# Performance work log

Measured on AMD Instinct MI355X. Metric: run time of the kernel, lower is better.

## Reference

```python
import jax, jax.numpy as jnp
import numpy as np

N_NODES = 100000
N_EDGES = 1600000
IN_CH, EDGE_DIM, HIDDEN, OUT_CH = 3, 3, 64, 1


def setup_inputs() -> dict:
    key = jax.random.key(0)
    ks = jax.random.split(key, 10)
    x = jax.random.normal(ks[0], (N_NODES, IN_CH), dtype=jnp.float32)
    edge_index = jax.random.randint(ks[1], (2, N_EDGES), 0, N_NODES, dtype=jnp.int64)
    edge_attr = jax.random.normal(ks[2], (N_EDGES, EDGE_DIM), dtype=jnp.float32)
    # Linear params (torch Linear: y = x @ W.T + b); we store W as (in, out)
    s1 = 1.0 / np.sqrt(IN_CH + EDGE_DIM)
    W1 = jax.random.uniform(ks[3], (IN_CH + EDGE_DIM, HIDDEN), jnp.float32, -s1, s1)
    b1 = jax.random.uniform(ks[4], (HIDDEN,), jnp.float32, -s1, s1)
    s2 = 1.0 / np.sqrt(HIDDEN + EDGE_DIM)
    W2 = jax.random.uniform(ks[5], (HIDDEN + EDGE_DIM, HIDDEN), jnp.float32, -s2, s2)
    b2 = jax.random.uniform(ks[6], (HIDDEN,), jnp.float32, -s2, s2)
    s3 = 1.0 / np.sqrt(HIDDEN)
    W3 = jax.random.uniform(ks[7], (HIDDEN, OUT_CH), jnp.float32, -s3, s3)
    b3 = jax.random.uniform(ks[8], (OUT_CH,), jnp.float32, -s3, s3)
    return {"x": x, "edge_index": edge_index, "edge_attr": edge_attr,
            "W1": W1, "b1": b1, "W2": W2, "b2": b2, "W3": W3, "b3": b3}


def _edge_conv(h, src, dst, edge_attr, W, b, n_nodes):
    # gather source node features, concat edge_attr, linear, scatter-add at dst
    msg = jnp.concatenate([h[src], edge_attr], axis=-1) @ W + b  # [E, out]
    return jax.ops.segment_sum(msg, dst, num_segments=n_nodes)   # [N, out]


def reference(x, edge_index, edge_attr, W1, b1, W2, b2, W3, b3):
    src, dst = edge_index[0], edge_index[1]  # PyG source_to_target: aggregate at edge_index[1]
    n = x.shape[0]
    h = jax.nn.relu(_edge_conv(x, src, dst, edge_attr, W1, b1, n))
    h = jax.nn.relu(_edge_conv(h, src, dst, edge_attr, W2, b2, n))
    return h @ W3 + b3  # (n_nodes, 1) anomaly logits
```

## Files before the change

### kernel.cpp

```cpp
#include <hip/hip_runtime.h>

#define N_NODES 100000
#define N_EDGES 1600000
#define NCHUNK 256
#define CHUNK_E (N_EDGES / NCHUNK)
#define BSHIFT 6
#define BMASK 63
#define NBUCK 1563
#define CAP 24
#define CSRB 1536
#define REC_CAP 1344


typedef unsigned int uint4_ev __attribute__((ext_vector_type(4)));
typedef short bf16x8 __attribute__((ext_vector_type(8)));
typedef float f32x4 __attribute__((ext_vector_type(4)));

__device__ __forceinline__ unsigned short f2bf(float f) {
    unsigned int u = __float_as_uint(f);
    unsigned int r = (u + 0x7fff + ((u >> 16) & 1)) >> 16;
    return (unsigned short)r;
}
__device__ __forceinline__ unsigned int pack2bf(float a, float b) {
    return (unsigned int)f2bf(a) | ((unsigned int)f2bf(b) << 16);
}
__device__ __forceinline__ float bflo(unsigned int v) { return __uint_as_float(v << 16); }
__device__ __forceinline__ float bfhi(unsigned int v) { return __uint_as_float(v & 0xffff0000u); }

__device__ __forceinline__ float4 nt_load4(const float4* p) {
    uint4_ev v = __builtin_nontemporal_load((const uint4_ev*)p);
    return make_float4(__uint_as_float(v.x), __uint_as_float(v.y),
                       __uint_as_float(v.z), __uint_as_float(v.w));
}

__device__ __forceinline__ int wave_incl_scan(int v, int lane) {
#pragma unroll
    for (int off = 1; off < 64; off <<= 1) {
        int t = __shfl_up(v, off, 64);
        if (lane >= off) v += t;
    }
    return v;
}

__global__ __launch_bounds__(1024) void k_scatter(const int* __restrict__ ei,
                                                  const float* __restrict__ ea,
                                                  const float* __restrict__ W2,
                                                  unsigned short* __restrict__ wpk,
                                                  const float* __restrict__ x,
                                                  float4* __restrict__ xp,
                                                  unsigned char* __restrict__ cnt8,
                                                  float4* __restrict__ stg) {
    const int g = blockIdx.x, t = threadIdx.x;
    if (g > NCHUNK) {
        int i = (g - NCHUNK - 1) * 1024 + t;
        if (i < N_NODES)
            xp[i] = make_float4(x[i * 3 + 0], x[i * 3 + 1], x[i * 3 + 2], 0.f);
        return;
    }
    if (g == NCHUNK) {
        if (t < 512) {
            int lane = t & 63, hh = (t >> 6) & 1, nt = t >> 7;
            int col = nt * 16 + (lane & 15);
            int k0 = hh * 32 + (lane >> 4) * 8;
#pragma unroll
            for (int j = 0; j < 8; j++)
                wpk[t * 8 + j] = f2bf(W2[(k0 + j) * 64 + col]);
        }
        return;
    }
    __shared__ int cur[NBUCK];
    for (int i = t; i < NBUCK; i += 1024) cur[i] = 0;
    const int base = g * CHUNK_E;
    int srcv[7], dstv[7];
    float a0v[7], a1v[7], a2v[7];
#pragma unroll
    for (int k = 0; k < 7; k++) {
        int i = t + k * 1024;
        if (i < CHUNK_E) {
            int e = base + i;
            srcv[k] = ei[e];
            dstv[k] = ei[N_EDGES + e];
            a0v[k] = ea[(size_t)e * 3 + 0];
            a1v[k] = ea[(size_t)e * 3 + 1];
            a2v[k] = ea[(size_t)e * 3 + 2];
        }
    }
    __syncthreads();
#pragma unroll
    for (int k = 0; k < 7; k++) {
        int i = t + k * 1024;
        if (i < CHUNK_E) {
            int bb = dstv[k] >> BSHIFT;
            int p = atomicAdd(&cur[bb], 1);
            if (p < CAP) {
                unsigned pk = (unsigned)srcv[k] | ((unsigned)(dstv[k] & BMASK) << 17);
                stg[((size_t)bb * NCHUNK + g) * CAP + p] =
                    make_float4(__uint_as_float(pk), a0v[k], a1v[k], a2v[k]);
            }
        }
    }
    __syncthreads();
    for (int i = t; i < NBUCK; i += 1024)
        cnt8[(size_t)g * NBUCK + i] = (unsigned char)min(cur[i], 255);
}

__global__ __launch_bounds__(512) void k_finalize(
    const float4* __restrict__ stg, const unsigned char* __restrict__ cnt8,
    const float4* __restrict__ xp, const float* __restrict__ W1,
    const float* __restrict__ b1, const float* __restrict__ W2,
    const float* __restrict__ b2, const bf16x8* __restrict__ wpk,
    int* __restrict__ csr, int* __restrict__ rowinfo,
    unsigned int* __restrict__ zu, unsigned int* __restrict__ eu) {
    __shared__ float4 rec[REC_CAP];
    __shared__ unsigned short stripof[REC_CAP];
    __shared__ int hist[64], lofs[64], curq[64];
    __shared__ float sU[64 * 3], sT[64 * 3];
    __shared__ int ws8[8];
    const int b = blockIdx.x, t = threadIdx.x;
    const int lane = t & 63, w = t >> 6;
    const int c = (t < NCHUNK) ? min((int)cnt8[(size_t)t * NBUCK + b], CAP) : 0;
    int inc = wave_incl_scan(c, lane);
    if (lane == 63) ws8[w] = inc;
    if (t < 64) hist[t] = 0;
    __syncthreads();
    int wo = 0;
#pragma unroll
    for (int k = 0; k < 8; k++) wo += (k < w) ? ws8[k] : 0;
    const int ex = wo + inc - c;
    int tot = 0;
#pragma unroll
    for (int k = 0; k < 8; k++) tot += ws8[k];
    const int cntb = min(tot, REC_CAP);
    for (int j = 0; j < c; ++j)
        if (ex + j < REC_CAP)
            stripof[ex + j] = (unsigned short)((t << 5) | j);
    __syncthreads();
    float4 r_[3];
#pragma unroll
    for (int k = 0; k < 3; k++) {
        int i = t + k * 512;
        if (i < cntb) {
            int sp = stripof[i];
            r_[k] = nt_load4(&stg[((size_t)b * NCHUNK + (sp >> 5)) * CAP + (sp & 31)]);
        }
    }
#pragma unroll
    for (int k = 0; k < 3; k++) {
        int i = t + k * 512;
        if (i < cntb) atomicAdd(&hist[__float_as_uint(r_[k].x) >> 17], 1);
    }
    __syncthreads();
    if (t < 64) {
        int v = hist[t];
        int in2 = wave_incl_scan(v, t);
        lofs[t] = in2 - v;
        curq[t] = in2 - v;
    }
    __syncthreads();
#pragma unroll
    for (int k = 0; k < 3; k++) {
        int i = t + k * 512;
        if (i < cntb) {
            int p = atomicAdd(&curq[__float_as_uint(r_[k].x) >> 17], 1);
            if (p < REC_CAP) rec[p] = r_[k];
        }
    }
    __syncthreads();
    {
        const int l = t >> 3, sub = t & 7;
        const int n = b * 64 + l;
        const int d = hist[l], lo = lofs[l];
        float u0 = 0, u1 = 0, u2 = 0, t0 = 0, t1 = 0, t2 = 0;
        for (int j = sub; j < d; j += 8) {
            float4 r = rec[lo + j];
            unsigned pk = __float_as_uint(r.x);
            int src = pk & 0x1FFFF;
            csr[b * CSRB + lo + j] = src;
            t0 += r.y; t1 += r.z; t2 += r.w;
            float4 xv = xp[src];
            u0 += xv.x; u1 += xv.y; u2 += xv.z;
        }
#pragma unroll
        for (int off = 1; off <= 4; off <<= 1) {
            u0 += __shfl_xor(u0, off, 64); u1 += __shfl_xor(u1, off, 64);
            u2 += __shfl_xor(u2, off, 64); t0 += __shfl_xor(t0, off, 64);
            t1 += __shfl_xor(t1, off, 64); t2 += __shfl_xor(t2, off, 64);
        }
        if (sub == 0) {
            sU[l * 3 + 0] = u0; sU[l * 3 + 1] = u1; sU[l * 3 + 2] = u2;
            sT[l * 3 + 0] = t0; sT[l * 3 + 1] = t1; sT[l * 3 + 2] = t2;
            if (n < N_NODES)
                rowinfo[n] = (int)(((unsigned)(b * CSRB + lo) << 8) | (unsigned)d);
        }
    }
    __syncthreads();
    if (w >= 4) return;
    const int tb = b * 64 + w * 16;
    if (tb >= N_NODES) return;
    const int col = lane & 15;
    const int q = lane >> 4;
    const int ln = w * 16 + col;
    const float d = (float)hist[ln];
    const float u0 = sU[ln * 3], u1 = sU[ln * 3 + 1], u2 = sU[ln * 3 + 2];
    const float t0 = sT[ln * 3], t1 = sT[ln * 3 + 1], t2 = sT[ln * 3 + 2];
    bf16x8 af[2];
#pragma unroll
    for (int h = 0; h < 2; h++) {
#pragma unroll
        for (int j = 0; j < 8; j++) {
            int cch = h * 32 + q * 8 + j;
            float a = d * b1[cch];
            a = fmaf(u0, W1[0 * 64 + cch], a);
            a = fmaf(u1, W1[1 * 64 + cch], a);
            a = fmaf(u2, W1[2 * 64 + cch], a);
            a = fmaf(t0, W1[3 * 64 + cch], a);
            a = fmaf(t1, W1[4 * 64 + cch], a);
            a = fmaf(t2, W1[5 * 64 + cch], a);
            af[h][j] = (short)f2bf(fmaxf(a, 0.f));
        }
    }
    f32x4 acc[4];
#pragma unroll
    for (int nt = 0; nt < 4; nt++) {
        bf16x8 b0 = wpk[(nt * 2 + 0) * 64 + lane];
        bf16x8 b1f = wpk[(nt * 2 + 1) * 64 + lane];
        f32x4 a = {0.f, 0.f, 0.f, 0.f};
        a = __builtin_amdgcn_mfma_f32_16x16x32_bf16(af[0], b0, a, 0, 0, 0);
        a = __builtin_amdgcn_mfma_f32_16x16x32_bf16(af[1], b1f, a, 0, 0, 0);
        acc[nt] = a;
    }
#pragma unroll
    for (int nt = 0; nt < 4; nt++) {
#pragma unroll
        for (int r = 0; r < 4; r++) {
            float v = acc[nt][r];
            float pv = __shfl_xor(v, 1, 64);
            if ((lane & 1) == 0) {
                int nr = tb + q * 4 + r;
                zu[(size_t)nr * 32 + nt * 8 + (col >> 1)] = pack2bf(v, pv);
            }
        }
    }
    const float eb = b2[lane];
    const float w64 = W2[64 * 64 + lane];
    const float w65 = W2[65 * 64 + lane];
    const float w66 = W2[66 * 64 + lane];
#pragma unroll 4
    for (int mm = 0; mm < 16; mm++) {
        int lm = w * 16 + mm;
        float dd = (float)hist[lm];
        float s0 = sT[lm * 3], s1 = sT[lm * 3 + 1], s2 = sT[lm * 3 + 2];
        float e = dd * eb;
        e = fmaf(s0, w64, e); e = fmaf(s1, w65, e); e = fmaf(s2, w66, e);
        float pe = __shfl_xor(e, 1, 64);
        if ((lane & 1) == 0)
            eu[(size_t)(tb + mm) * 32 + (lane >> 1)] = pack2bf(e, pe);
    }
}

__global__ __launch_bounds__(256) void k_agg(
    const unsigned int* __restrict__ zu, const unsigned int* __restrict__ eu,
    const int* __restrict__ rowinfo, const int* __restrict__ csr,
    const float* __restrict__ W3, const float* __restrict__ b3,
    float* __restrict__ out) {
    const int lane = threadIdx.x & 63;
    const int li = lane & 15;
    const int q = li & 7;
    const int r = li >> 3;
    const int n = blockIdx.x * 16 + (threadIdx.x >> 4);

    float cw3[8];
#pragma unroll
    for (int m = 0; m < 8; m++) cw3[m] = W3[8 * q + m];
    const float b3v = b3[0];

    const unsigned ri = (unsigned)rowinfo[n];
    const int start = (int)(ri >> 8), end = start + (int)(ri & 255u);
    float S[8];
#pragma unroll
    for (int m = 0; m < 8; m++) S[m] = 0.f;

    for (int c = start; c < end; c += 16) {
        int idx[8];
        float mk[8];
        uint4 v[8];
#pragma unroll
        for (int u = 0; u < 8; u++) {
            int i = c + 2 * u + r;
            bool ok = i < end;
            mk[u] = ok ? 1.f : 0.f;
            idx[u] = csr[ok ? i : start];
        }
#pragma unroll
        for (int u = 0; u < 8; u++)
            v[u] = *(const uint4*)&zu[(size_t)idx[u] * 32 + q * 4];
#pragma unroll
        for (int u = 0; u < 8; u++) {
            S[0] = fmaf(mk[u], bflo(v[u].x), S[0]); S[1] = fmaf(mk[u], bfhi(v[u].x), S[1]);
            S[2] = fmaf(mk[u], bflo(v[u].y), S[2]); S[3] = fmaf(mk[u], bfhi(v[u].y), S[3]);
            S[4] = fmaf(mk[u], bflo(v[u].z), S[4]); S[5] = fmaf(mk[u], bfhi(v[u].z), S[5]);
            S[6] = fmaf(mk[u], bflo(v[u].w), S[6]); S[7] = fmaf(mk[u], bfhi(v[u].w), S[7]);
        }
    }
#pragma unroll
    for (int m = 0; m < 8; m++) S[m] += __shfl_xor(S[m], 8, 64);

    const uint4 ev = *(const uint4*)&eu[(size_t)n * 32 + q * 4];
    float contrib;
    {
        float h0 = fmaxf(S[0] + bflo(ev.x), 0.f);
        float h1v = fmaxf(S[1] + bfhi(ev.x), 0.f);
        float h2v = fmaxf(S[2] + bflo(ev.y), 0.f);
        float h3 = fmaxf(S[3] + bfhi(ev.y), 0.f);
        float h4 = fmaxf(S[4] + bflo(ev.z), 0.f);
        float h5 = fmaxf(S[5] + bfhi(ev.z), 0.f);
        float h6 = fmaxf(S[6] + bflo(ev.w), 0.f);
        float h7 = fmaxf(S[7] + bfhi(ev.w), 0.f);
        contrib = h0 * cw3[0];
        contrib = fmaf(h1v, cw3[1], contrib);
        contrib = fmaf(h2v, cw3[2], contrib);
        contrib = fmaf(h3, cw3[3], contrib);
        contrib = fmaf(h4, cw3[4], contrib);
        contrib = fmaf(h5, cw3[5], contrib);
        contrib = fmaf(h6, cw3[6], contrib);
        contrib = fmaf(h7, cw3[7], contrib);
    }
    contrib += __shfl_xor(contrib, 1, 64);
    contrib += __shfl_xor(contrib, 2, 64);
    contrib += __shfl_xor(contrib, 4, 64);
    if (li == 0) out[n] = contrib + b3v;
}

extern "C" void kernel_launch(void* const* d_in, const int* in_sizes, int n_in,
                              void* d_out, int out_size, void* d_ws, size_t ws_size,
                              hipStream_t stream) {
    const float* x  = (const float*)d_in[0];
    const int*   ei = (const int*)d_in[1];
    const float* ea = (const float*)d_in[2];
    const float* W1 = (const float*)d_in[3];
    const float* b1 = (const float*)d_in[4];
    const float* W2 = (const float*)d_in[5];
    const float* b2 = (const float*)d_in[6];
    const float* W3 = (const float*)d_in[7];
    const float* b3 = (const float*)d_in[8];
    float* out = (float*)d_out;

    char* ws = (char*)d_ws;
    unsigned char* cnt8 = (unsigned char*)(ws + 0);
    int*    rowinfo = (int*)(ws + 400128);
    int*    csr     = (int*)(ws + 800128);
    unsigned int* zu = (unsigned int*)(ws + 10403200);
    unsigned int* eu = (unsigned int*)(ws + 23203200);
    unsigned short* wpk = (unsigned short*)(ws + 36003200);
    float4* xp  = (float4*)(ws + 36011392);
    float4* stg = (float4*)(ws + 37611392);

    k_scatter<<<NCHUNK + 99, 1024, 0, stream>>>(ei, ea, W2, wpk, x, xp, cnt8, stg);
    k_finalize<<<NBUCK, 512, 0, stream>>>(stg, cnt8, xp, W1, b1, W2, b2,
                                          (const bf16x8*)wpk, csr, rowinfo, zu, eu);
    k_agg<<<N_NODES / 16, 256, 0, stream>>>(zu, eu, rowinfo, csr, W3, b3, out);
}
```

Before: 168.7 us.

## Split each scatter chunk into two half-chunk blocks with separate staging slots

The edge-bucketing scatter kernel now launches two blocks per edge chunk, each handling half the edges with its own 14-slot staging region and its own count row. The finalize kernel reads 512 sub-chunk counts instead of 256 and decodes the new staging addresses. The aim is more parallelism and fewer registers per thread in the scatter phase on a GPU with many CUs. In exchange there are more count bytes to write and read, and the total staging capacity grows from 24 to 28 slots per chunk, which adds memory footprint and could shift overflow behaviour.

```diff
diff --git a/kernel.cpp b/kernel.cpp
--- a/kernel.cpp
+++ b/kernel.cpp
@@ -4,10 +4,12 @@
 #define N_EDGES 1600000
 #define NCHUNK 256
 #define CHUNK_E (N_EDGES / NCHUNK)
+#define HALF_E (CHUNK_E / 2)
 #define BSHIFT 6
 #define BMASK 63
 #define NBUCK 1563
-#define CAP 24
+#define HCAP 14
+#define CAP 28
 #define CSRB 1536
 #define REC_CAP 1344
 
@@ -50,33 +52,34 @@
                                                   float4* __restrict__ xp,
                                                   unsigned char* __restrict__ cnt8,
                                                   float4* __restrict__ stg) {
-    const int g = blockIdx.x, t = threadIdx.x;
-    if (g > NCHUNK) {
-        int i = (g - NCHUNK - 1) * 1024 + t;
+    const int j = blockIdx.x, t = threadIdx.x;
+    if (j > 2 * NCHUNK) {
+        int i = (j - 2 * NCHUNK - 1) * 1024 + t;
         if (i < N_NODES)
             xp[i] = make_float4(x[i * 3 + 0], x[i * 3 + 1], x[i * 3 + 2], 0.f);
         return;
     }
-    if (g == NCHUNK) {
+    if (j == 2 * NCHUNK) {
         if (t < 512) {
             int lane = t & 63, hh = (t >> 6) & 1, nt = t >> 7;
             int col = nt * 16 + (lane & 15);
             int k0 = hh * 32 + (lane >> 4) * 8;
 #pragma unroll
-            for (int j = 0; j < 8; j++)
-                wpk[t * 8 + j] = f2bf(W2[(k0 + j) * 64 + col]);
+            for (int jj = 0; jj < 8; jj++)
+                wpk[t * 8 + jj] = f2bf(W2[(k0 + jj) * 64 + col]);
         }
         return;
     }
+    const int g = j >> 1, h = j & 1;
     __shared__ int cur[NBUCK];
     for (int i = t; i < NBUCK; i += 1024) cur[i] = 0;
-    const int base = g * CHUNK_E;
-    int srcv[7], dstv[7];
-    float a0v[7], a1v[7], a2v[7];
-#pragma unroll
-    for (int k = 0; k < 7; k++) {
+    const int base = g * CHUNK_E + h * HALF_E;
+    int srcv[4], dstv[4];
+    float a0v[4], a1v[4], a2v[4];
+#pragma unroll
+    for (int k = 0; k < 4; k++) {
         int i = t + k * 1024;
-        if (i < CHUNK_E) {
+        if (i < HALF_E) {
             int e = base + i;
             srcv[k] = ei[e];
             dstv[k] = ei[N_EDGES + e];
@@ -87,21 +90,21 @@
     }
     __syncthreads();
 #pragma unroll
-    for (int k = 0; k < 7; k++) {
+    for (int k = 0; k < 4; k++) {
         int i = t + k * 1024;
-        if (i < CHUNK_E) {
+        if (i < HALF_E) {
             int bb = dstv[k] >> BSHIFT;
             int p = atomicAdd(&cur[bb], 1);
-            if (p < CAP) {
+            if (p < HCAP) {
                 unsigned pk = (unsigned)srcv[k] | ((unsigned)(dstv[k] & BMASK) << 17);
-                stg[((size_t)bb * NCHUNK + g) * CAP + p] =
+                stg[((size_t)bb * NCHUNK + g) * CAP + h * HCAP + p] =
                     make_float4(__uint_as_float(pk), a0v[k], a1v[k], a2v[k]);
             }
         }
     }
     __syncthreads();
     for (int i = t; i < NBUCK; i += 1024)
-        cnt8[(size_t)g * NBUCK + i] = (unsigned char)min(cur[i], 255);
+        cnt8[(size_t)(2 * g + h) * NBUCK + i] = (unsigned char)min(cur[i], 255);
 }
 
 __global__ __launch_bounds__(512) void k_finalize(
@@ -118,7 +121,7 @@
     __shared__ int ws8[8];
     const int b = blockIdx.x, t = threadIdx.x;
     const int lane = t & 63, w = t >> 6;
-    const int c = (t < NCHUNK) ? min((int)cnt8[(size_t)t * NBUCK + b], CAP) : 0;
+    const int c = min((int)cnt8[(size_t)t * NBUCK + b], HCAP);
     int inc = wave_incl_scan(c, lane);
     if (lane == 63) ws8[w] = inc;
     if (t < 64) hist[t] = 0;
@@ -133,7 +136,7 @@
     const int cntb = min(tot, REC_CAP);
     for (int j = 0; j < c; ++j)
         if (ex + j < REC_CAP)
-            stripof[ex + j] = (unsigned short)((t << 5) | j);
+            stripof[ex + j] = (unsigned short)((t << 4) | j);
     __syncthreads();
     float4 r_[3];
 #pragma unroll
@@ -141,7 +144,9 @@
         int i = t + k * 512;
         if (i < cntb) {
             int sp = stripof[i];
-            r_[k] = nt_load4(&stg[((size_t)b * NCHUNK + (sp >> 5)) * CAP + (sp & 31)]);
+            int vc = sp >> 4;
+            r_[k] = nt_load4(&stg[((size_t)b * NCHUNK + (vc >> 1)) * CAP +
+                                  (vc & 1) * HCAP + (sp & 15)]);
         }
     }
 #pragma unroll
@@ -347,15 +352,15 @@
 
     char* ws = (char*)d_ws;
     unsigned char* cnt8 = (unsigned char*)(ws + 0);
-    int*    rowinfo = (int*)(ws + 400128);
-    int*    csr     = (int*)(ws + 800128);
-    unsigned int* zu = (unsigned int*)(ws + 10403200);
-    unsigned int* eu = (unsigned int*)(ws + 23203200);
-    unsigned short* wpk = (unsigned short*)(ws + 36003200);
-    float4* xp  = (float4*)(ws + 36011392);
-    float4* stg = (float4*)(ws + 37611392);
-
-    k_scatter<<<NCHUNK + 99, 1024, 0, stream>>>(ei, ea, W2, wpk, x, xp, cnt8, stg);
+    int*    rowinfo = (int*)(ws + 800256);
+    int*    csr     = (int*)(ws + 1200384);
+    unsigned int* zu = (unsigned int*)(ws + 10803456);
+    unsigned int* eu = (unsigned int*)(ws + 23603456);
+    unsigned short* wpk = (unsigned short*)(ws + 36403456);
+    float4* xp  = (float4*)(ws + 36411648);
+    float4* stg = (float4*)(ws + 38011648);
+
+    k_scatter<<<2 * NCHUNK + 100, 1024, 0, stream>>>(ei, ea, W2, wpk, x, xp, cnt8, stg);
     k_finalize<<<NBUCK, 512, 0, stream>>>(stg, cnt8, xp, W1, b1, W2, b2,
                                           (const bf16x8*)wpk, csr, rowinfo, zu, eu);
     k_agg<<<N_NODES / 16, 256, 0, stream>>>(zu, eu, rowinfo, csr, W3, b3, out);
```

After: 178.1 us. +5.5%, slower.
